# Kernel optimization log

Hardware: AMD Instinct MI355X
Metric: run time of the kernel (lower is better)

Reference implementation:

```python
import jax, jax.numpy as jnp
import numpy as np
from jax import lax

T, B, I, H = 2048, 64, 256, 256  # seq_len, batch, input_size, hidden_size


def setup_inputs() -> dict:
    key = jax.random.key(0)
    k1, k2, k3, k4 = jax.random.split(key, 4)
    scale = 1.0 / np.sqrt(H)  # ~ torch Linear default init magnitude
    x = jax.random.normal(k1, (T, B, I), dtype=jnp.float32)
    w_in = jax.random.normal(k2, (4 * H, I), dtype=jnp.float32) * scale
    b = jax.random.normal(k3, (4 * H,), dtype=jnp.float32) * scale
    w_rec = jax.random.normal(k4, (4 * H, H), dtype=jnp.float32) * scale
    return {"x": x, "w_in": w_in, "b": b, "w_rec": w_rec}


def reference(x, w_in, b, w_rec):
    # x: [T, B, I] (batch_first=False). Single-layer vanilla subLSTM.
    # Precompute input projection for all timesteps (one big GEMM).
    gx = jnp.einsum('tbi,gi->tbg', x, w_in) + b  # [T, B, 4H]
    h0 = jnp.zeros((x.shape[1], w_rec.shape[1]), dtype=x.dtype)
    c0 = jnp.zeros_like(h0)

    def cell(carry, gxt):
        h, c = carry
        gates = jax.nn.sigmoid(gxt + h @ w_rec.T)  # all 4 gates sigmoid
        i_g, o_g, z_g, f_g = jnp.split(gates, 4, axis=-1)
        c_new = f_g * c + z_g - i_g          # subtractive input gate
        h_new = jax.nn.sigmoid(c_new) - o_g  # subtractive output gate
        return (h_new, c_new), h_new

    (h_last, c_last), outputs = lax.scan(cell, (h0, c0), gx)
    return outputs  # [T, B, H]
```

## Files before the change

kernel.cpp:

```cpp
#include <hip/hip_runtime.h>
#include <cstdint>
#include <cstddef>

typedef __attribute__((ext_vector_type(8))) short short8;
typedef __attribute__((ext_vector_type(4))) float f32x4;
typedef __attribute__((ext_vector_type(4))) unsigned int u32x4;
typedef __attribute__((ext_vector_type(4))) int i32x4;

#define NEG_LOG2E -1.44269504088896340736f
#define MFMA_BF16 __builtin_amdgcn_mfma_f32_16x16x32_bf16
#define MFMA_I8 __builtin_amdgcn_mfma_i32_16x16x64_i8
#define CH 256

static __device__ __forceinline__ unsigned int cvt_pk_bf16(float lo, float hi) {
  unsigned int r;
  asm("v_cvt_pk_bf16_f32 %0, %1, %2" : "=v"(r) : "v"(lo), "v"(hi));
  return r;
}
static __device__ __forceinline__ float sigmoid_scaled(float xs) {
  return __builtin_amdgcn_rcpf(1.0f + __builtin_amdgcn_exp2f(xs));
}

#define GMF8_BODY                                        \
  "v_mfma_f32_16x16x32_bf16 %0, %8, %12, %0\n\t"         \
  "v_mfma_f32_16x16x32_bf16 %1, %8, %13, %1\n\t"         \
  "v_mfma_f32_16x16x32_bf16 %2, %9, %12, %2\n\t"         \
  "v_mfma_f32_16x16x32_bf16 %3, %9, %13, %3\n\t"         \
  "v_mfma_f32_16x16x32_bf16 %4, %10, %12, %4\n\t"        \
  "v_mfma_f32_16x16x32_bf16 %5, %10, %13, %5\n\t"        \
  "v_mfma_f32_16x16x32_bf16 %6, %11, %12, %6\n\t"        \
  "v_mfma_f32_16x16x32_bf16 %7, %11, %13, %7"
#define GMF8_OUTS                                                          \
  "+&a"(c00), "+&a"(c01), "+&a"(c10), "+&a"(c11), "+&a"(c20), "+&a"(c21),  \
  "+&a"(c30), "+&a"(c31)
#define GMF8_INS                                                           \
  "v"(a0), "v"(a1), "v"(a2), "v"(a3), "v"(b0), "v"(b1)
#define DEF_GMF8(name, lead, tail)                                         \
  static __device__ __forceinline__ void name(                             \
      short8 a0, short8 a1, short8 a2, short8 a3, short8 b0, short8 b1,    \
      f32x4& c00, f32x4& c01, f32x4& c10, f32x4& c11, f32x4& c20,          \
      f32x4& c21, f32x4& c30, f32x4& c31) {                                \
    asm(lead GMF8_BODY tail : GMF8_OUTS : GMF8_INS);                       \
  }
DEF_GMF8(gmf8_first, "s_nop 3\n\t", "")
DEF_GMF8(gmf8_mid, "", "")
DEF_GMF8(gmf8_last, "", "\n\ts_nop 7\n\ts_nop 7\n\ts_nop 3")

__global__ void wscale_setup(const float* __restrict__ w_rec,
                             float* __restrict__ scbuf,
                             float* __restrict__ w127) {
  const int j = blockIdx.x;
  const int l = threadIdx.x;
  const float* row = w_rec + (size_t)j * 256;
  float m = 0.f;
#pragma unroll
  for (int k = 0; k < 4; ++k) m = fmaxf(m, fabsf(row[l + 64 * k]));
#pragma unroll
  for (int d = 32; d > 0; d >>= 1) m = fmaxf(m, __shfl_xor(m, d));
  if (l == 0) {
    float s = fmaxf(m * 1.44269504088896f, 1e-30f);
    scbuf[j] = s / 16129.0f;
    w127[j] = 127.0f / s;
  }
}

__global__ void wfrag_setup_i8(const float* __restrict__ w_rec,
                               const float* __restrict__ w127,
                               unsigned int* __restrict__ wfq) {
  const int f = blockIdx.x;
  const int l = threadIdx.x;
  const int w = f >> 6, q = f & 63;
  const int chain = q >> 2, kt = q & 3;
  const int jidx = chain >> 2, g = chain & 3;
  const int jt = (jidx < 2) ? (2 * w + jidx) : (2 * w + 8 + (jidx - 2));
  const int ct = jt + 16 * g;
  const int j = ct * 16 + (l & 15);
  const float r = w127[j];
  const float* src = w_rec + (size_t)j * 256 + kt * 64 + (l >> 4) * 16;
  u32x4 ov;
#pragma unroll
  for (int d = 0; d < 4; ++d) {
    unsigned int word = 0;
#pragma unroll
    for (int e = 0; e < 4; ++e) {
      int qi = (int)rintf(src[4 * d + e] * NEG_LOG2E * r);
      qi = qi > 127 ? 127 : (qi < -127 ? -127 : qi);
      word |= ((unsigned int)(qi & 255)) << (8 * e);
    }
    ov[d] = word;
  }
  *(u32x4*)(wfq + (size_t)f * 256 + (size_t)l * 4) = ov;
}

static __device__ __forceinline__ short8 ldcvt8(const float* p) {
  f32x4 v0 = *(const f32x4*)p;
  f32x4 v1 = *(const f32x4*)(p + 4);
  u32x4 u;
  u[0] = cvt_pk_bf16(v0[0], v0[1]);
  u[1] = cvt_pk_bf16(v0[2], v0[3]);
  u[2] = cvt_pk_bf16(v1[0], v1[1]);
  u[3] = cvt_pk_bf16(v1[2], v1[3]);
  return __builtin_bit_cast(short8, u);
}

__global__ __launch_bounds__(256) void gemm_gx(const float* __restrict__ x,
                                               const float* __restrict__ w_in,
                                               const float* __restrict__ bias,
                                               unsigned int* __restrict__ gx) {
  const int n = blockIdx.x;
  const int bx = (n >> 3) & 7;
  const int by = (n >> 6) * 8 + (n & 7);
  const int l = threadIdx.x & 63, wid = threadIdx.x >> 6;
  const int mq = wid >> 1, nq = wid & 1;
  const int mbase = by * 128 + mq * 64;
  const int nbase = bx * 128 + nq * 64;
  const int lr = l & 15;
  const int lk = (l >> 4) * 8;

  f32x4 acc[4][4] = {};
#pragma unroll
  for (int kt = 0; kt < 8; ++kt) {
    const int k0 = kt * 32 + lk;
    short8 af[4], bf[4];
#pragma unroll
    for (int mt = 0; mt < 4; ++mt)
      af[mt] = ldcvt8(x + (size_t)(mbase + mt * 16 + lr) * 256 + k0);
#pragma unroll
    for (int nt = 0; nt < 4; ++nt)
      bf[nt] = ldcvt8(w_in + (size_t)(nbase + nt * 16 + lr) * 256 + k0);
#pragma unroll
    for (int mt = 0; mt < 4; ++mt)
#pragma unroll
      for (int nt = 0; nt < 4; ++nt)
        acc[mt][nt] = MFMA_BF16(af[mt], bf[nt], acc[mt][nt], 0, 0, 0);
  }

  float bv[4];
#pragma unroll
  for (int nt = 0; nt < 4; ++nt) bv[nt] = bias[nbase + nt * 16 + lr];

#pragma unroll
  for (int mt = 0; mt < 4; ++mt) {
    const int m0 = mbase + mt * 16;
    const int tt = m0 >> 6;
    const int bg = ((m0 & 63) >> 2) + (l >> 4);
#pragma unroll
    for (int ntp = 0; ntp < 2; ++ntp) {
      const int p = (nbase >> 5) + ntp;
      const int pb = p & 7, g = p >> 3;
#pragma unroll
      for (int r = 0; r < 4; ++r) {
        float e0 = (acc[mt][ntp * 2 + 0][r] + bv[ntp * 2 + 0]) * NEG_LOG2E;
        float e1 = (acc[mt][ntp * 2 + 1][r] + bv[ntp * 2 + 1]) * NEG_LOG2E;
        gx[(((((size_t)tt * 16 + bg) * 8 + pb) * 64) + (r * 16 + lr)) * 4 + g] =
            cvt_pk_bf16(e0, e1);
      }
    }
  }
}

#define HB8_ROW 288
#define HB8_SZ (4 * HB8_ROW)
#define LDS_TOTAL (2 * HB8_SZ)

#define LD4A(i)                                                         \
  asm volatile("global_load_dwordx4 %0, %4, off\n\t"                    \
               "global_load_dwordx4 %1, %4, off offset:1024\n\t"        \
               "global_load_dwordx4 %2, %4, off offset:2048\n\t"        \
               "global_load_dwordx4 %3, %4, off offset:3072"            \
               : "=&a"(wa[4 * (i)]), "=&a"(wa[4 * (i) + 1]),            \
                 "=&a"(wa[4 * (i) + 2]), "=&a"(wa[4 * (i) + 3])         \
               : "v"(pA + 4096 * (i)))

__global__ __launch_bounds__(1024) void scan_gemm(
    const unsigned int* __restrict__ wfq, const float* __restrict__ scbuf,
    const unsigned int* __restrict__ gx, float* __restrict__ out,
    float* __restrict__ hstate, float* __restrict__ cstate, int first,
    const float* __restrict__ xn, const float* __restrict__ w_in,
    const float* __restrict__ bias, unsigned int* __restrict__ gxn,
    int do_gemm) {
  if (blockIdx.x >= 16) {
    if (!do_gemm) return;
    const int mm = blockIdx.x - 16;
    const int by = mm >> 2;
    const int sub = threadIdx.x >> 8;
    const int strip = ((mm & 3) << 2) + sub;
    const int tix = threadIdx.x & 255;
    const int l = tix & 63, wid = tix >> 6;
    const int mq = wid >> 1, nq = wid & 1;
    const int mbase = by * 128 + mq * 64;
    const int nbase = strip * 64 + nq * 32;
    const int lr = l & 15, lk = (l >> 4) * 8;

    f32x4 c00 = {0.f, 0.f, 0.f, 0.f}, c01 = c00, c10 = c00, c11 = c00;
    f32x4 c20 = c00, c21 = c00, c30 = c00, c31 = c00;
#pragma unroll
    for (int kt = 0; kt < 8; ++kt) {
      const int k0 = kt * 32 + lk;
      const short8 a0 = ldcvt8(xn + (size_t)(mbase + 0 * 16 + lr) * 256 + k0);
      const short8 a1 = ldcvt8(xn + (size_t)(mbase + 1 * 16 + lr) * 256 + k0);
      const short8 a2 = ldcvt8(xn + (size_t)(mbase + 2 * 16 + lr) * 256 + k0);
      const short8 a3 = ldcvt8(xn + (size_t)(mbase + 3 * 16 + lr) * 256 + k0);
      const short8 b0 = ldcvt8(w_in + (size_t)(nbase + 0 * 16 + lr) * 256 + k0);
      const short8 b1 = ldcvt8(w_in + (size_t)(nbase + 1 * 16 + lr) * 256 + k0);
      if (kt == 0)
        gmf8_first(a0, a1, a2, a3, b0, b1, c00, c01, c10, c11, c20, c21, c30, c31);
      else if (kt < 7)
        gmf8_mid(a0, a1, a2, a3, b0, b1, c00, c01, c10, c11, c20, c21, c30, c31);
      else
        gmf8_last(a0, a1, a2, a3, b0, b1, c00, c01, c10, c11, c20, c21, c30, c31);
    }

    const float bv0 = bias[nbase + lr];
    const float bv1 = bias[nbase + 16 + lr];
    const int p = nbase >> 5;
    const int pb = p & 7, g = p >> 3;
    const f32x4* accm[4][2] = {{&c00, &c01}, {&c10, &c11},
                               {&c20, &c21}, {&c30, &c31}};
#pragma unroll
    for (int mt = 0; mt < 4; ++mt) {
      const int m0 = mbase + mt * 16;
      const int tt = m0 >> 6;
      const int bg = ((m0 & 63) >> 2) + (l >> 4);
#pragma unroll
      for (int r = 0; r < 4; ++r) {
        float e0 = ((*accm[mt][0])[r] + bv0) * NEG_LOG2E;
        float e1 = ((*accm[mt][1])[r] + bv1) * NEG_LOG2E;
        gxn[(((((size_t)tt * 16 + bg) * 8 + pb) * 64) + (r * 16 + lr)) * 4 + g] =
            cvt_pk_bf16(e0, e1);
      }
    }
    return;
  }

  extern __shared__ char lds[];
  char* hb0 = lds;
  char* hb1 = lds + HB8_SZ;

  const int l = threadIdx.x & 63;
  const int w = threadIdx.x >> 6;
  const int bg = blockIdx.x;
  const int bloc = l >> 4;
  const int col = l & 15;
  const int jt = w;
  const int fbase = (jt < 8) ? ((jt >> 1) * 64 + (jt & 1) * 16)
                             : (((jt - 8) >> 1) * 64 + (2 + (jt & 1)) * 16);

  i32x4 wa[16];
  {
    const char* pA = (const char*)wfq + (size_t)fbase * 1024 + (size_t)l * 16;
    LD4A(0); LD4A(1); LD4A(2); LD4A(3);
    asm volatile("s_waitcnt vmcnt(0)" ::: "memory");
  }
  float scv[4];
#pragma unroll
  for (int g = 0; g < 4; ++g)
    scv[g] = scbuf[(jt + 16 * g) * 16 + col];

  float carr;
  if (first) {
    for (int i = threadIdx.x; i < (2 * HB8_SZ) / 4; i += 1024)
      ((unsigned int*)hb0)[i] = 0u;
    carr = 0.0f;
  } else {
    const size_t idx = (size_t)(bg * 4 + bloc) * 256 + jt * 16 + col;
    carr = cstate[idx];
    const int qi = (int)rintf(hstate[idx] * 127.f);
    *(char*)(hb0 + bloc * HB8_ROW + jt * 16 + col) = (char)qi;
  }

  u32x4 gxA, gxB;
  {
    const unsigned int* g0 =
        gx + ((((size_t)0 * 16 + bg) * 8 + (jt >> 1)) << 8) + 4 * l;
    gxA = *(const u32x4*)g0;
  }
  __syncthreads();

  float* outp = out + (size_t)(bg * 4 + bloc) * 256 + col + jt * 16;
  const int aoff = ((l & 15) >> 2) * HB8_ROW + (l >> 4) * 16;
  const int hwoff = bloc * HB8_ROW;
  const bool hi = (jt & 1) != 0;

  auto STEP = [&](int t, char* hbR, char* hbW, u32x4& gxC, u32x4& gxN) {
    const int tn = (t + 1 < CH) ? (t + 1) : (CH - 1);
    const unsigned int* gn =
        gx + ((((size_t)tn * 16 + bg) * 8 + (jt >> 1)) << 8) + 4 * l;
    gxN = *(const u32x4*)gn;

    const char* hrd = hbR + aoff;
    i32x4 afv[4];
#pragma unroll
    for (int kt = 0; kt < 4; ++kt)
      afv[kt] = *(const i32x4*)(hrd + kt * 64);

    i32x4 d0 = {0, 0, 0, 0}, d1 = d0, d2 = d0, d3 = d0;
#pragma unroll
    for (int kt = 0; kt < 4; ++kt) {
      d0 = MFMA_I8(afv[kt], wa[kt], d0, 0, 0, 0);
      d1 = MFMA_I8(afv[kt], wa[4 + kt], d1, 0, 0, 0);
      d2 = MFMA_I8(afv[kt], wa[8 + kt], d2, 0, 0, 0);
      d3 = MFMA_I8(afv[kt], wa[12 + kt], d3, 0, 0, 0);
    }

    {
      const float g0f = hi ? __uint_as_float(gxC[0] & 0xffff0000u)
                           : __uint_as_float(gxC[0] << 16);
      const float g1f = hi ? __uint_as_float(gxC[1] & 0xffff0000u)
                           : __uint_as_float(gxC[1] << 16);
      const float g2f = hi ? __uint_as_float(gxC[2] & 0xffff0000u)
                           : __uint_as_float(gxC[2] << 16);
      const float g3f = hi ? __uint_as_float(gxC[3] & 0xffff0000u)
                           : __uint_as_float(gxC[3] << 16);
      const float gi = sigmoid_scaled(fmaf((float)d0[0], scv[0], g0f));
      const float go = sigmoid_scaled(fmaf((float)d1[0], scv[1], g1f));
      const float gz = sigmoid_scaled(fmaf((float)d2[0], scv[2], g2f));
      const float gf = sigmoid_scaled(fmaf((float)d3[0], scv[3], g3f));
      carr = gf * carr + (gz - gi);
      const float hs = sigmoid_scaled(carr * NEG_LOG2E);
      const float hn = hs - go;
      outp[(size_t)t * 16384] = hn;
      const int qh = (int)rintf(hn * 127.f);
      *(char*)(hbW + hwoff + jt * 16 + col) = (char)qh;
    }

    __builtin_amdgcn_sched_barrier(0);
    asm volatile("s_waitcnt lgkmcnt(0)");
    __builtin_amdgcn_s_barrier();
    __builtin_amdgcn_sched_barrier(0);
  };

  for (int tt = 0; tt < CH / 2; ++tt) {
    STEP(2 * tt, hb0, hb1, gxA, gxB);
    STEP(2 * tt + 1, hb1, hb0, gxB, gxA);
  }

  {
    const size_t idx = (size_t)(bg * 4 + bloc) * 256 + jt * 16 + col;
    const signed char qv =
        *(const signed char*)(hb0 + hwoff + jt * 16 + col);
    hstate[idx] = (float)qv / 127.f;
    cstate[idx] = carr;
  }
}

extern "C" void kernel_launch(void* const* d_in, const int* in_sizes, int n_in,
                              void* d_out, int out_size, void* d_ws,
                              size_t ws_size, hipStream_t stream) {
  const float* x = (const float*)d_in[0];
  const float* w_in = (const float*)d_in[1];
  const float* bias = (const float*)d_in[2];
  const float* wrec = (const float*)d_in[3];
  float* out = (float*)d_out;
  char* ws = (char*)d_ws;

  unsigned int* wfq = (unsigned int*)ws;
  float* scbuf = (float*)(ws + (256 << 10));
  float* w127 = (float*)(ws + (260 << 10));
  float* hstate = (float*)(ws + (512 << 10));
  float* cstate = (float*)(ws + (576 << 10));
  unsigned int* gxb[2] = {(unsigned int*)(ws + (1ull << 20)),
                          (unsigned int*)(ws + (33ull << 20))};

  (void)in_sizes; (void)n_in; (void)out_size; (void)ws_size;

  wscale_setup<<<dim3(1024), dim3(64), 0, stream>>>(wrec, scbuf, w127);
  wfrag_setup_i8<<<dim3(256), dim3(64), 0, stream>>>(wrec, w127, wfq);

  const size_t chelt = (size_t)CH * 64 * 256;
  gemm_gx<<<dim3(1024), dim3(256), 0, stream>>>(x, w_in, bias, gxb[0]);

  for (int c = 0; c < 8; ++c) {
    const int nxt = (c + 1 < 8) ? (c + 1) : 0;
    scan_gemm<<<dim3(16 + 512), dim3(1024), LDS_TOTAL, stream>>>(
        wfq, scbuf, gxb[c & 1], out + (size_t)c * chelt, hstate, cstate,
        (c == 0) ? 1 : 0, x + (size_t)nxt * chelt, w_in, bias,
        gxb[(c + 1) & 1], (c < 7) ? 1 : 0);
  }
}
```

Before: 1.720 ms.

## Fuse weight-scale computation into fragment setup and enlarge scan LDS allocation

Removes the separate wscale_setup launch by computing each row's max-abs scale inside wfrag_setup_i8, which saves one kernel launch at the cost of redundant row reads across blocks. The dynamic LDS request for scan_gemm is raised to 80 KiB via hipFuncSetAttribute, likely to limit co-resident blocks per CU so the persistent scan blocks are not crowded by GEMM blocks. The larger LDS request may reduce occupancy for the gemm part of the same kernel.

```diff
diff --git a/kernel.cpp b/kernel.cpp
--- a/kernel.cpp
+++ b/kernel.cpp
@@ -46,26 +46,8 @@
 DEF_GMF8(gmf8_mid, "", "")
 DEF_GMF8(gmf8_last, "", "\n\ts_nop 7\n\ts_nop 7\n\ts_nop 3")
 
-__global__ void wscale_setup(const float* __restrict__ w_rec,
-                             float* __restrict__ scbuf,
-                             float* __restrict__ w127) {
-  const int j = blockIdx.x;
-  const int l = threadIdx.x;
-  const float* row = w_rec + (size_t)j * 256;
-  float m = 0.f;
-#pragma unroll
-  for (int k = 0; k < 4; ++k) m = fmaxf(m, fabsf(row[l + 64 * k]));
-#pragma unroll
-  for (int d = 32; d > 0; d >>= 1) m = fmaxf(m, __shfl_xor(m, d));
-  if (l == 0) {
-    float s = fmaxf(m * 1.44269504088896f, 1e-30f);
-    scbuf[j] = s / 16129.0f;
-    w127[j] = 127.0f / s;
-  }
-}
-
 __global__ void wfrag_setup_i8(const float* __restrict__ w_rec,
-                               const float* __restrict__ w127,
+                               float* __restrict__ scbuf,
                                unsigned int* __restrict__ wfq) {
   const int f = blockIdx.x;
   const int l = threadIdx.x;
@@ -75,8 +57,18 @@
   const int jt = (jidx < 2) ? (2 * w + jidx) : (2 * w + 8 + (jidx - 2));
   const int ct = jt + 16 * g;
   const int j = ct * 16 + (l & 15);
-  const float r = w127[j];
-  const float* src = w_rec + (size_t)j * 256 + kt * 64 + (l >> 4) * 16;
+  const float* row = w_rec + (size_t)j * 256;
+
+  float m = 0.f;
+#pragma unroll
+  for (int k = 0; k < 64; ++k) m = fmaxf(m, fabsf(row[(l >> 4) * 64 + k]));
+  m = fmaxf(m, __shfl_xor(m, 16));
+  m = fmaxf(m, __shfl_xor(m, 32));
+  const float s = fmaxf(m * 1.44269504088896f, 1e-30f);
+  const float r = 127.0f / s;
+  if ((l >> 4) == 0 && kt == 0) scbuf[j] = s / 16129.0f;
+
+  const float* src = row + kt * 64 + (l >> 4) * 16;
   u32x4 ov;
 #pragma unroll
   for (int d = 0; d < 4; ++d) {
@@ -161,7 +153,7 @@
 
 #define HB8_ROW 288
 #define HB8_SZ (4 * HB8_ROW)
-#define LDS_TOTAL (2 * HB8_SZ)
+#define LDS_ALLOC (80 * 1024)
 
 #define LD4A(i)                                                         \
   asm volatile("global_load_dwordx4 %0, %4, off\n\t"                    \
@@ -356,7 +348,6 @@
 
   unsigned int* wfq = (unsigned int*)ws;
   float* scbuf = (float*)(ws + (256 << 10));
-  float* w127 = (float*)(ws + (260 << 10));
   float* hstate = (float*)(ws + (512 << 10));
   float* cstate = (float*)(ws + (576 << 10));
   unsigned int* gxb[2] = {(unsigned int*)(ws + (1ull << 20)),
@@ -364,15 +355,17 @@
 
   (void)in_sizes; (void)n_in; (void)out_size; (void)ws_size;
 
-  wscale_setup<<<dim3(1024), dim3(64), 0, stream>>>(wrec, scbuf, w127);
-  wfrag_setup_i8<<<dim3(256), dim3(64), 0, stream>>>(wrec, w127, wfq);
+  hipFuncSetAttribute((const void*)scan_gemm,
+                      hipFuncAttributeMaxDynamicSharedMemorySize, LDS_ALLOC);
+
+  wfrag_setup_i8<<<dim3(256), dim3(64), 0, stream>>>(wrec, scbuf, wfq);
 
   const size_t chelt = (size_t)CH * 64 * 256;
   gemm_gx<<<dim3(1024), dim3(256), 0, stream>>>(x, w_in, bias, gxb[0]);
 
   for (int c = 0; c < 8; ++c) {
     const int nxt = (c + 1 < 8) ? (c + 1) : 0;
-    scan_gemm<<<dim3(16 + 512), dim3(1024), LDS_TOTAL, stream>>>(
+    scan_gemm<<<dim3(16 + 512), dim3(1024), LDS_ALLOC, stream>>>(
         wfq, scbuf, gxb[c & 1], out + (size_t)c * chelt, hstate, cstate,
         (c == 0) ? 1 : 0, x + (size_t)nxt * chelt, w_in, bias,
         gxb[(c + 1) & 1], (c < 7) ? 1 : 0);
```

Measured after the change: 1.721 ms. No clear change (+0.0%).
